# Kernel optimization log

Measured on AMD Instinct MI355X. Metric: run time of the kernel, lower is better.

Reference implementation:

```python
import jax, jax.numpy as jnp
import numpy as np

N = 20000      # nodes
E = 80000      # edges (before self loops)
NG = 64        # graphs in batch
EMB = 780      # embedding_size (768 text + 12 time)
NEG_SLOPE = 0.2
BN_EPS = 1e-5


def setup_inputs() -> dict:
    key = jax.random.key(0)
    ks = jax.random.split(key, 20)
    def rn(k, shape, s=0.05):
        return jax.random.normal(k, shape, dtype=jnp.float32) * s
    z = lambda n: jnp.zeros((n,), dtype=jnp.float32)
    o = lambda n: jnp.ones((n,), dtype=jnp.float32)
    x = jax.random.normal(ks[0], (N, 772), dtype=jnp.float32)
    edge_index = jax.random.randint(ks[1], (2, E), 0, N)
    batch = jnp.sort(jax.random.randint(ks[2], (N,), 0, NG))
    return dict(
        x=x, edge_index=edge_index, batch=batch,
        time_W=rn(ks[3], (4, 12)), time_b=z(12),
        lin_W0=rn(ks[4], (EMB, 3 * EMB)), att_src0=rn(ks[5], (3, EMB)), att_dst0=rn(ks[6], (3, EMB)),
        bias0=z(3 * EMB), gamma0=o(3 * EMB), beta0=z(3 * EMB),
        lin_W1=rn(ks[7], (3 * EMB, 3 * EMB)), att_src1=rn(ks[8], (3, EMB)), att_dst1=rn(ks[9], (3, EMB)),
        bias1=z(3 * EMB), gamma1=o(3 * EMB), beta1=z(3 * EMB),
        lin_W2=rn(ks[10], (3 * EMB, EMB)), att_src2=rn(ks[11], (1, EMB)), att_dst2=rn(ks[12], (1, EMB)),
        bias2=z(EMB), gamma2=o(EMB), beta2=z(EMB),
        mlp_W1=rn(ks[13], (EMB, 128)), mlp_b1=z(128),
        mlp_W2=rn(ks[14], (128, 64)), mlp_b2=z(64),
    )


def _gat_layer(h, src, dst, W, a_src, a_dst, b, heads):
    # PyG GATConv (eval mode: dropout off), concat=True, self loops already in src/dst
    C = W.shape[1] // heads
    hp = (h @ W).reshape(N, heads, C)                       # [N,H,C]
    a_s = jnp.sum(hp * a_src[None], axis=-1)                # [N,H]
    a_d = jnp.sum(hp * a_dst[None], axis=-1)                # [N,H]
    e = jax.nn.leaky_relu(a_s[src] + a_d[dst], NEG_SLOPE)   # [E+N,H]
    m = jax.ops.segment_max(e, dst, num_segments=N)         # segment softmax over incoming edges
    m = jnp.where(jnp.isfinite(m), m, 0.0)
    p = jnp.exp(e - m[dst])
    denom = jax.ops.segment_sum(p, dst, num_segments=N)
    alpha = p / (denom[dst] + 1e-16)                        # [E+N,H]
    out = jax.ops.segment_sum(alpha[:, :, None] * hp[src], dst, num_segments=N)  # [N,H,C]
    return out.reshape(N, heads * C) + b


def _bn(h, gamma, beta):
    # BatchNorm in training-mode math (batch statistics, biased variance)
    mu = jnp.mean(h, axis=0)
    var = jnp.mean((h - mu) ** 2, axis=0)
    return (h - mu) * jax.lax.rsqrt(var + BN_EPS) * gamma + beta


def reference(x, edge_index, batch, time_W, time_b,
              lin_W0, att_src0, att_dst0, bias0, gamma0, beta0,
              lin_W1, att_src1, att_dst1, bias1, gamma1, beta1,
              lin_W2, att_src2, att_dst2, bias2, gamma2, beta2,
              mlp_W1, mlp_b1, mlp_W2, mlp_b2):
    te = x[:, 768:772] @ time_W + time_b
    h = jnp.concatenate([jax.lax.stop_gradient(x[:, :768]), te,
                         jax.lax.stop_gradient(x[:, 772:])], axis=-1)  # [N, 780]
    sl = jnp.arange(N)
    src = jnp.concatenate([edge_index[0], sl])   # add self loops
    dst = jnp.concatenate([edge_index[1], sl])
    layers = [
        (lin_W0, att_src0, att_dst0, bias0, gamma0, beta0, 3),
        (lin_W1, att_src1, att_dst1, bias1, gamma1, beta1, 3),
        (lin_W2, att_src2, att_dst2, bias2, gamma2, beta2, 1),
    ]
    for W, a_s, a_d, b, g, bt, heads in layers:
        h = jnp.tanh(_gat_layer(h, src, dst, W, a_s, a_d, b, heads))
        h = _bn(h, g, bt)
    cnt = jax.ops.segment_sum(jnp.ones((N,), dtype=h.dtype), batch, num_segments=NG)
    pooled = jax.ops.segment_sum(h, batch, num_segments=NG) / jnp.maximum(cnt, 1.0)[:, None]
    pooled = jax.nn.relu(pooled)
    out = jnp.tanh(pooled @ mlp_W1 + mlp_b1) @ mlp_W2 + mlp_b2
    return out  # [NG, 64]
```

## Files before the change

kernel.cpp:

```cpp
#include <hip/hip_runtime.h>
#include <math.h>

#define NN   20000
#define EE   80000
#define ELP  100000
#define NGR  64
#define EMB  780
#define W3   2340
#define EMBP 832
#define W3P  2368

static inline int cdiv_i(long long a, long long b){ return (int)((a + b - 1) / b); }

typedef _Float16 f16;
typedef _Float16 f16x4 __attribute__((ext_vector_type(4)));
typedef _Float16 f16x8 __attribute__((ext_vector_type(8)));
typedef float    f32x4 __attribute__((ext_vector_type(4)));

__device__ __forceinline__ void async_ld16(const f16* g, f16* l){
    __builtin_amdgcn_global_load_lds(
        (const __attribute__((address_space(1))) unsigned int*)g,
        (__attribute__((address_space(3))) unsigned int*)l,
        16, 0, 0);
}

__global__ void k_zero_f32(float* p, int n){
    int i = blockIdx.x*256 + threadIdx.x; if (i < n) p[i] = 0.f;
}
__global__ void k_zero_i32(int* p, int n){
    int i = blockIdx.x*256 + threadIdx.x; if (i < n) p[i] = 0;
}
__global__ void k_copy_i32(const int* __restrict__ s, int* __restrict__ d, int n){
    int i = blockIdx.x*256 + threadIdx.x; if (i < n) d[i] = s[i];
}

__global__ void k_transpose(const float* __restrict__ W, f16* __restrict__ Wt,
                            const float* __restrict__ sc, int K, int N, int KP){
    __shared__ float T[32][33];
    int n0 = blockIdx.x*32, k0 = blockIdx.y*32;
    int tx = threadIdx.x, ty = threadIdx.y;
#pragma unroll
    for (int r = 0; r < 4; r++){
        int k = k0 + ty + r*8;
        float v = 0.f;
        if (k < K && n0 + tx < N){
            v = W[(size_t)k*N + n0 + tx];
            if (sc) v *= sc[k];
        }
        T[ty + r*8][tx] = v;
    }
    __syncthreads();
#pragma unroll
    for (int r = 0; r < 4; r++){
        int n = n0 + ty + r*8;
        int k = k0 + tx;
        if (n < N && k < KP) Wt[(size_t)n*KP + k] = (f16)T[tx][ty + r*8];
    }
}

#define DVEC_KSPLIT 32
__global__ void k_dvec(const float* __restrict__ W, const float* __restrict__ sh,
                       float* __restrict__ dvec, int K, int N){
    int n = blockIdx.x*256 + threadIdx.x;
    if (n >= N) return;
    int slice = blockIdx.y;
    int k0 = (int)(((long long)K * slice) / DVEC_KSPLIT);
    int k1 = (int)(((long long)K * (slice+1)) / DVEC_KSPLIT);
    float s = 0.f;
    for (int k = k0; k < k1; k++) s += sh[k] * W[(size_t)k*N + n];
    atomicAdd(&dvec[n], s);
}

__global__ void k_build_h(const float* __restrict__ x, const float* __restrict__ tW,
                          const float* __restrict__ tb, f16* __restrict__ h){
    int idx = blockIdx.x*256 + threadIdx.x;
    if (idx >= NN*EMBP) return;
    int n = idx / EMBP, c = idx - n*EMBP;
    const float* xr = x + (size_t)n*772;
    float v;
    if (c < 768) v = xr[c];
    else if (c < EMB){
        int j = c - 768;
        v = tb[j] + xr[768]*tW[j] + xr[769]*tW[12+j] + xr[770]*tW[24+j] + xr[771]*tW[36+j];
    } else v = 0.f;
    h[idx] = (f16)v;
}

__global__ void k_deg(const int* __restrict__ ei, int* __restrict__ deg){
    int k = blockIdx.x*256 + threadIdx.x; if (k >= ELP) return;
    int d = (k < EE) ? ei[EE + k] : (k - EE);
    atomicAdd(&deg[d], 1);
}

__global__ __launch_bounds__(1024) void k_scan(const int* __restrict__ deg, int* __restrict__ rp){
    __shared__ int part[1024];
    int tid = threadIdx.x;
    int i0 = tid*20;
    int n = (i0 < NN) ? min(20, NN - i0) : 0;
    int s = 0;
    for (int k = 0; k < n; k++) s += deg[i0+k];
    part[tid] = s; __syncthreads();
    for (int off = 1; off < 1024; off <<= 1){
        int t = (tid >= off) ? part[tid-off] : 0;
        __syncthreads();
        part[tid] += t;
        __syncthreads();
    }
    int run = part[tid] - s;
    for (int k = 0; k < n; k++){ rp[i0+k] = run; run += deg[i0+k]; }
    if (tid == 1023) rp[NN] = part[1023];
}

__global__ void k_fill(const int* __restrict__ ei, int* __restrict__ cursor, int* __restrict__ csrc){
    int k = blockIdx.x*256 + threadIdx.x; if (k >= ELP) return;
    int s, d;
    if (k < EE){ s = ei[k]; d = ei[EE + k]; } else { s = k - EE; d = s; }
    int pos = atomicAdd(&cursor[d], 1);
    csrc[pos] = s;
}

__global__ void k_grp(const int* __restrict__ batch, int* __restrict__ grp){
    int g = blockIdx.x*256 + threadIdx.x; if (g > NGR) return;
    int lo = 0, hi = NN;
    while (lo < hi){ int mid = (lo+hi)>>1; if (batch[mid] < g) lo = mid+1; else hi = mid; }
    grp[g] = lo;
}

__global__ __launch_bounds__(256) void k_gemm_mfma(const f16* __restrict__ A,
                                                   const f16* __restrict__ Bt,
                                                   const float* __restrict__ dvec,
                                                   f16* __restrict__ C,
                                                   int M, int N, int KP, int SN,
                                                   int Mtiles, int NT){
    int bid = blockIdx.x;
    int xcd = bid & 7;
    int j   = bid >> 3;
    int sl  = j / NT;
    int nt  = j - sl*NT;
    int mt  = sl*8 + xcd;
    if (mt >= Mtiles) return;
    int m0 = mt*128, n0 = nt*128;

    __shared__ f16 As[128*64];
    __shared__ f16 Bs[128*64];
    int tid = threadIdx.x;
    int w = tid >> 6, lane = tid & 63;

    int lrow = lane >> 2;
    int lko  = (lane & 3) * 8;

    int i2a = w*2, i2b = w*2 + 1;
    const f16* gA0 = A  + (size_t)min(m0 + i2a*16 + lrow, M-1)*KP + lko;
    const f16* gA1 = A  + (size_t)min(m0 + i2b*16 + lrow, M-1)*KP + lko;
    const f16* gB0 = Bt + (size_t)min(n0 + i2a*16 + lrow, N-1)*KP + lko;
    const f16* gB1 = Bt + (size_t)min(n0 + i2b*16 + lrow, N-1)*KP + lko;
    f16* lA0 = &As[i2a*512]; f16* lA1 = &As[i2b*512];
    f16* lB0 = &Bs[i2a*512]; f16* lB1 = &Bs[i2b*512];

    f32x4 acc[4][4];
#pragma unroll
    for (int i = 0; i < 4; i++)
#pragma unroll
        for (int j2 = 0; j2 < 4; j2++) acc[i][j2] = (f32x4)0.f;

    int wm = (w & 1) * 64, wn = (w >> 1) * 64;
    int lq = lane >> 4, lm = lane & 15;

    for (int kk = 0; kk < KP; kk += 64){
        __syncthreads();
        async_ld16(gA0 + kk, lA0);
        async_ld16(gA1 + kk, lA1);
        async_ld16(gB0 + kk, lB0);
        async_ld16(gB1 + kk, lB1);
        async_ld16(gA0 + kk + 32, lA0 + 4096);
        async_ld16(gA1 + kk + 32, lA1 + 4096);
        async_ld16(gB0 + kk + 32, lB0 + 4096);
        async_ld16(gB1 + kk + 32, lB1 + 4096);
        __syncthreads();

#pragma unroll
        for (int half = 0; half < 2; half++){
            const f16* Ap = As + half*4096;
            const f16* Bp = Bs + half*4096;
            f16x8 aF[4], bF[4];
#pragma unroll
            for (int mi = 0; mi < 4; mi++)
                aF[mi] = *(const f16x8*)&Ap[(wm + mi*16 + lm)*32 + lq*8];
#pragma unroll
            for (int ni = 0; ni < 4; ni++)
                bF[ni] = *(const f16x8*)&Bp[(wn + ni*16 + lm)*32 + lq*8];
#pragma unroll
            for (int mi = 0; mi < 4; mi++)
#pragma unroll
                for (int ni = 0; ni < 4; ni++)
                    acc[mi][ni] = __builtin_amdgcn_mfma_f32_16x16x32_f16(aF[mi], bF[ni], acc[mi][ni], 0, 0, 0);
        }
    }

#pragma unroll
    for (int mi = 0; mi < 4; mi++){
#pragma unroll
        for (int ni = 0; ni < 4; ni++){
            int col = n0 + wn + ni*16 + lm;
            if (col < SN){
                float dv = (col < N) ? dvec[col] : 0.f;
                int rbase = m0 + wm + mi*16 + lq*4;
#pragma unroll
                for (int r = 0; r < 4; r++){
                    int row = rbase + r;
                    if (row < M){
                        float v = (col < N) ? (acc[mi][ni][r] + dv) : 0.f;
                        C[(size_t)row*SN + col] = (f16)v;
                    }
                }
            }
        }
    }
}

__global__ void k_att(const f16* __restrict__ hp, const float* __restrict__ asrc,
                      const float* __restrict__ adst, float* __restrict__ a_s,
                      float* __restrict__ a_d, int H, int SP){
    int n = blockIdx.x;
    int wv = threadIdx.x >> 6, lane = threadIdx.x & 63;
    const f16* row = hp + (size_t)n*SP + wv*EMB;
    const float* pa = asrc + wv*EMB;
    const float* pd = adst + wv*EMB;
    float s = 0.f, d = 0.f;
    for (int c = lane*4; c < EMB; c += 256){
        f16x4 v = *(const f16x4*)(row + c);
#pragma unroll
        for (int jj = 0; jj < 4; jj++){
            float f = (float)v[jj];
            s += f*pa[c+jj]; d += f*pd[c+jj];
        }
    }
#pragma unroll
    for (int off = 32; off; off >>= 1){ s += __shfl_xor(s, off); d += __shfl_xor(d, off); }
    if (lane == 0){ a_s[n*H + wv] = s; a_d[n*H + wv] = d; }
}

template<int H>
__global__ __launch_bounds__(256) void k_agg2(const f16* __restrict__ hp, const int* __restrict__ rp,
                                              const int* __restrict__ csrc, const float* __restrict__ a_s,
                                              const float* __restrict__ a_d, const float* __restrict__ bias,
                                              f16* __restrict__ y, int SP, int W){
    int n = blockIdx.x, tid = threadIdx.x, lane = tid & 63;
    int beg = rp[n], deg = rp[n+1] - beg;

    float adv[H];
#pragma unroll
    for (int h = 0; h < H; h++) adv[h] = a_d[n*H + h];

    float mx[H];
#pragma unroll
    for (int h = 0; h < H; h++) mx[h] = -1e30f;
    for (int base = 0; base < deg; base += 64){
        int e = base + lane;
        if (e < deg){
            int s = csrc[beg + e];
#pragma unroll
            for (int h = 0; h < H; h++){
                float t = a_s[s*H + h] + adv[h];
                t = t > 0.f ? t : 0.2f*t;
                mx[h] = fmaxf(mx[h], t);
            }
        }
    }
#pragma unroll
    for (int off = 32; off; off >>= 1)
#pragma unroll
        for (int h = 0; h < H; h++) mx[h] = fmaxf(mx[h], __shfl_xor(mx[h], off));

    float dn[H];
#pragma unroll
    for (int h = 0; h < H; h++) dn[h] = 0.f;
    for (int base = 0; base < deg; base += 64){
        int e = base + lane;
        if (e < deg){
            int s = csrc[beg + e];
#pragma unroll
            for (int h = 0; h < H; h++){
                float t = a_s[s*H + h] + adv[h];
                t = t > 0.f ? t : 0.2f*t;
                dn[h] += expf(t - mx[h]);
            }
        }
    }
#pragma unroll
    for (int off = 32; off; off >>= 1)
#pragma unroll
        for (int h = 0; h < H; h++) dn[h] += __shfl_xor(dn[h], off);
    float inv[H];
#pragma unroll
    for (int h = 0; h < H; h++) inv[h] = 1.f / (dn[h] + 1e-16f);

    float acc[2][8];
#pragma unroll
    for (int g = 0; g < 2; g++)
#pragma unroll
        for (int j = 0; j < 8; j++) acc[g][j] = 0.f;
    int  cg[2];  cg[0] = tid*8; cg[1] = 2048 + tid*8;
    bool act[2]; act[0] = cg[0] < W; act[1] = cg[1] < W;
    int hlo[2], hhi[2], nsp[2];
#pragma unroll
    for (int g = 0; g < 2; g++){
        int c = cg[g];
        int hl = min(c / EMB, H-1);
        int hh = min((c+7) / EMB, H-1);
        hlo[g] = hl; hhi[g] = hh;
        nsp[g] = (hh > hl) ? (EMB*(hl+1) - c) : 8;
    }

    for (int base = 0; base < deg; base += 64){
        int cnt = min(64, deg - base);
        int sl = 0; float al[H];
        {
            int e = base + lane;
            if (e < deg){
                sl = csrc[beg + e];
#pragma unroll
                for (int h = 0; h < H; h++){
                    float t = a_s[sl*H + h] + adv[h];
                    t = t > 0.f ? t : 0.2f*t;
                    al[h] = expf(t - mx[h]) * inv[h];
                }
            } else {
#pragma unroll
                for (int h = 0; h < H; h++) al[h] = 0.f;
            }
        }
#pragma unroll 2
        for (int e = 0; e < cnt; e++){
            int s = __shfl(sl, e);
            float a0 = __shfl(al[0], e);
            float a1 = (H==3) ? __shfl(al[1], e) : a0;
            float a2 = (H==3) ? __shfl(al[2], e) : a0;
            const f16* row = hp + (size_t)s*SP;
#pragma unroll
            for (int g = 0; g < 2; g++){
                if (act[g]){
                    f16x8 v = *(const f16x8*)(row + cg[g]);
                    float lo = (hlo[g]==0) ? a0 : (hlo[g]==1 ? a1 : a2);
                    float hi = (hhi[g]==0) ? a0 : (hhi[g]==1 ? a1 : a2);
#pragma unroll
                    for (int j = 0; j < 8; j++){
                        float alj = (j < nsp[g]) ? lo : hi;
                        acc[g][j] += alj * (float)v[j];
                    }
                }
            }
        }
    }

#pragma unroll
    for (int g = 0; g < 2; g++){
        int c = cg[g];
        if (c < SP){
            f16x8 o;
#pragma unroll
            for (int j = 0; j < 8; j++){
                float vv = (c + j < W) ? tanhf(acc[g][j] + bias[c+j]) : 0.f;
                o[j] = (f16)vv;
            }
            *(f16x8*)(y + (size_t)n*SP + c) = o;
        }
    }
}

__global__ void k_bnstat(const f16* __restrict__ y, float* __restrict__ ps,
                         float* __restrict__ pq, int W, int SP){
    int c0 = (blockIdx.x*256 + threadIdx.x)*4;
    if (c0 >= W) return;
    int slice = blockIdx.y;
    float s[4] = {0,0,0,0}, q[4] = {0,0,0,0};
    for (int r = slice; r < NN; r += 64){
        f16x4 u = *(const f16x4*)(y + (size_t)r*SP + c0);
#pragma unroll
        for (int j = 0; j < 4; j++){ float v = (float)u[j]; s[j] += v; q[j] += v*v; }
    }
#pragma unroll
    for (int j = 0; j < 4; j++){
        ps[(size_t)slice*W3 + c0+j] = s[j];
        pq[(size_t)slice*W3 + c0+j] = q[j];
    }
}

__global__ void k_bnfin(const float* __restrict__ ps, const float* __restrict__ pq,
                        const float* __restrict__ gamma, const float* __restrict__ beta,
                        float* __restrict__ sc, float* __restrict__ sh, int W){
    int c = blockIdx.x*256 + threadIdx.x; if (c >= W) return;
    float m = 0.f, q = 0.f;
    for (int s = 0; s < 64; s++){ m += ps[(size_t)s*W3 + c]; q += pq[(size_t)s*W3 + c]; }
    m *= (1.f/NN);
    float v = q * (1.f/NN) - m*m;
    float is = 1.f / sqrtf(v + 1e-5f);
    float g = gamma[c];
    sc[c] = is * g;
    sh[c] = beta[c] - m * is * g;
}

__global__ void k_pool(const f16* __restrict__ h, const int* __restrict__ grp,
                       float* __restrict__ pooled){
    int g = blockIdx.x;
    int c = threadIdx.x*4;
    if (c >= EMB) return;
    int r0 = grp[g], r1 = grp[g+1];
    float s0=0.f, s1=0.f, s2=0.f, s3=0.f;
    for (int r = r0; r < r1; r++){
        f16x4 u = *(const f16x4*)(h + (size_t)r*EMBP + c);
        s0 += (float)u[0]; s1 += (float)u[1]; s2 += (float)u[2]; s3 += (float)u[3];
    }
    pooled[g*EMB + c] = s0; pooled[g*EMB + c+1] = s1;
    pooled[g*EMB + c+2] = s2; pooled[g*EMB + c+3] = s3;
}

__global__ __launch_bounds__(256) void k_mlp(const float* __restrict__ pooled, const int* __restrict__ grp,
                                             const float* __restrict__ sc, const float* __restrict__ sh,
                                             const float* __restrict__ W1, const float* __restrict__ b1,
                                             const float* __restrict__ W2, const float* __restrict__ b2,
                                             float* __restrict__ out){
    __shared__ float p[EMB];
    __shared__ float hid[128];
    int g = blockIdx.x, tid = threadIdx.x;
    int cnt = grp[g+1] - grp[g];
    float ic = 1.f / fmaxf((float)cnt, 1.f);
    for (int c = tid; c < EMB; c += 256){
        float v = pooled[g*EMB + c] * ic * sc[c] + sh[c];
        p[c] = v > 0.f ? v : 0.f;
    }
    __syncthreads();
    if (tid < 128){
        float s = b1[tid];
        for (int k = 0; k < EMB; k++) s += p[k] * W1[k*128 + tid];
        hid[tid] = tanhf(s);
    }
    __syncthreads();
    if (tid < 64){
        float s = b2[tid];
        for (int k = 0; k < 128; k++) s += hid[k] * W2[k*64 + tid];
        out[g*64 + tid] = s;
    }
}

extern "C" void kernel_launch(void* const* d_in, const int* in_sizes, int n_in,
                              void* d_out, int out_size, void* d_ws, size_t ws_size,
                              hipStream_t stream) {
    (void)in_sizes; (void)n_in; (void)out_size;
    const float* x    = (const float*)d_in[0];
    const int*   ei   = (const int*)  d_in[1];
    const int*   batch= (const int*)  d_in[2];
    const float* tW   = (const float*)d_in[3];
    const float* tb   = (const float*)d_in[4];
    const float* W0   = (const float*)d_in[5];
    const float* as0  = (const float*)d_in[6];
    const float* ad0  = (const float*)d_in[7];
    const float* b0   = (const float*)d_in[8];
    const float* g0   = (const float*)d_in[9];
    const float* be0  = (const float*)d_in[10];
    const float* W1   = (const float*)d_in[11];
    const float* as1  = (const float*)d_in[12];
    const float* ad1  = (const float*)d_in[13];
    const float* b1   = (const float*)d_in[14];
    const float* g1   = (const float*)d_in[15];
    const float* be1  = (const float*)d_in[16];
    const float* W2   = (const float*)d_in[17];
    const float* as2  = (const float*)d_in[18];
    const float* ad2  = (const float*)d_in[19];
    const float* b2   = (const float*)d_in[20];
    const float* g2   = (const float*)d_in[21];
    const float* be2  = (const float*)d_in[22];
    const float* mW1  = (const float*)d_in[23];
    const float* mb1  = (const float*)d_in[24];
    const float* mW2  = (const float*)d_in[25];
    const float* mb2  = (const float*)d_in[26];
    float* outp = (float*)d_out;

    size_t off = 0;
    auto carve = [&](size_t bytes) -> void* {
        void* p = (char*)d_ws + off;
        off = (off + bytes + 255) & ~(size_t)255;
        return p;
    };
    f16* big1 = (f16*)carve((size_t)NN*W3P*2);
    f16* big2 = (f16*)carve((size_t)NN*W3P*2);
    f16* Wt   = (f16*)carve((size_t)W3*W3P*2);
    float* a_s   = (float*)carve((size_t)NN*3*4);
    float* a_d   = (float*)carve((size_t)NN*3*4);
    float* psum  = (float*)carve((size_t)64*W3*4);
    float* psq   = (float*)carve((size_t)64*W3*4);
    float* sc    = (float*)carve((size_t)W3*4);
    float* sh    = (float*)carve((size_t)W3*4);
    float* dvec  = (float*)carve((size_t)W3*4);
    float* pooled= (float*)carve((size_t)NGR*EMB*4);
    int*   grp   = (int*)carve((size_t)(NGR+1)*4);
    int*   deg   = (int*)carve((size_t)NN*4);
    int*   rp    = (int*)carve((size_t)(NN+1)*4);
    int*   csrc  = (int*)carve((size_t)ELP*4);

    if (ws_size < off) return;

    k_zero_i32<<<cdiv_i(NN,256),256,0,stream>>>(deg, NN);
    k_deg<<<cdiv_i(ELP,256),256,0,stream>>>(ei, deg);
    k_scan<<<1,1024,0,stream>>>(deg, rp);
    k_copy_i32<<<cdiv_i(NN,256),256,0,stream>>>(rp, deg, NN);
    k_fill<<<cdiv_i(ELP,256),256,0,stream>>>(ei, deg, csrc);
    k_grp<<<1,256,0,stream>>>(batch, grp);

    k_build_h<<<cdiv_i((long long)NN*EMBP,256),256,0,stream>>>(x, tW, tb, big1);

    struct Layer { const float* W; const float* as; const float* ad; const float* b;
                   const float* g; const float* be; int H; int K; int KP; };
    Layer layers[3] = {
        {W0, as0, ad0, b0, g0, be0, 3, EMB, EMBP},
        {W1, as1, ad1, b1, g1, be1, 3, W3,  W3P },
        {W2, as2, ad2, b2, g2, be2, 1, W3,  W3P },
    };

    for (int L = 0; L < 3; L++){
        Layer& ly = layers[L];
        int Wout  = ly.H * EMB;
        int SPout = (Wout == W3) ? W3P : EMBP;
        const float* scale = (L == 0) ? nullptr : sc;

        dim3 tg(cdiv_i(Wout,32), cdiv_i(ly.KP,32));
        k_transpose<<<tg, dim3(32,8), 0, stream>>>(ly.W, Wt, scale, ly.K, Wout, ly.KP);
        k_zero_f32<<<cdiv_i(W3,256),256,0,stream>>>(dvec, W3);
        if (L > 0){
            dim3 dg(cdiv_i(Wout,256), DVEC_KSPLIT);
            k_dvec<<<dg,256,0,stream>>>(ly.W, sh, dvec, ly.K, Wout);
        }

        int Mtiles = cdiv_i(NN,128), NT = cdiv_i(Wout,128);
        int nb = ((Mtiles+7)/8)*8*NT;
        k_gemm_mfma<<<nb, 256, 0, stream>>>(big1, Wt, dvec, big2, NN, Wout, ly.KP, SPout, Mtiles, NT);

        k_att<<<NN, ly.H*64, 0, stream>>>(big2, ly.as, ly.ad, a_s, a_d, ly.H, SPout);

        if (ly.H == 3)
            k_agg2<3><<<NN,256,0,stream>>>(big2, rp, csrc, a_s, a_d, ly.b, big1, SPout, Wout);
        else
            k_agg2<1><<<NN,256,0,stream>>>(big2, rp, csrc, a_s, a_d, ly.b, big1, SPout, Wout);

        dim3 gs(cdiv_i(Wout/4,256), 64);
        k_bnstat<<<gs,256,0,stream>>>(big1, psum, psq, Wout, SPout);
        k_bnfin<<<cdiv_i(Wout,256),256,0,stream>>>(psum, psq, ly.g, ly.be, sc, sh, Wout);
    }

    k_pool<<<NGR,256,0,stream>>>(big1, grp, pooled);
    k_mlp<<<NGR,256,0,stream>>>(pooled, grp, sc, sh, mW1, mb1, mW2, mb2, outp);
}
```

Before: 1.678 ms.

## Fold attention score projections into the GEMM as extra output columns

Precomputes W·a_src and W·a_dst vectors, including the BN scale, and appends them as extra rows of the transposed weight. The main MFMA GEMM then emits the per-node attention logits directly into a compact a_sd buffer, and the separate k_att pass that re-read the whole projected feature matrix is removed. The BN shift contribution is added through extended dvec entries computed by a tiny k_wfin kernel. The BN-stat row split also goes from 64 to 128 slices, and dvec zeroing is merged into k_bnfin. The attention logits now come from f16-rounded weight vectors instead of dot products over the stored features, which slightly changes precision.

```diff
diff --git a/kernel.cpp b/kernel.cpp
--- a/kernel.cpp
+++ b/kernel.cpp
@@ -9,6 +9,7 @@
 #define W3   2340
 #define EMBP 832
 #define W3P  2368
+#define NZ   (W3+8)
 
 static inline int cdiv_i(long long a, long long b){ return (int)((a + b - 1) / b); }
 
@@ -55,6 +56,46 @@
         int n = n0 + ty + r*8;
         int k = k0 + tx;
         if (n < N && k < KP) Wt[(size_t)n*KP + k] = (f16)T[tx][ty + r*8];
+    }
+}
+
+__global__ void k_wvec(const float* __restrict__ W, const float* __restrict__ asrc,
+                       const float* __restrict__ adst, const float* __restrict__ sc,
+                       f16* __restrict__ Wt, int K, int N, int KP, int H){
+    int k = blockIdx.x*4 + (threadIdx.x >> 6);
+    int lane = threadIdx.x & 63;
+    if (k >= K) return;
+    const float* row = W + (size_t)k*N;
+    float acc[6];
+#pragma unroll
+    for (int i = 0; i < 6; i++) acc[i] = 0.f;
+    for (int c = lane; c < EMB; c += 64){
+        for (int h = 0; h < H; h++){
+            float wv = row[h*EMB + c];
+            acc[h]     += wv * asrc[h*EMB + c];
+            acc[H + h] += wv * adst[h*EMB + c];
+        }
+    }
+    float s = sc ? sc[k] : 1.f;
+    for (int i = 0; i < 2*H; i++){
+        float v = acc[i];
+#pragma unroll
+        for (int off = 32; off; off >>= 1) v += __shfl_xor(v, off);
+        if (lane == 0) Wt[(size_t)(N + i)*KP + k] = (f16)(v * s);
+    }
+}
+
+__global__ void k_wfin(const float* __restrict__ asrc, const float* __restrict__ adst,
+                       float* __restrict__ dvec, int N, int H){
+    int wv = threadIdx.x >> 6, lane = threadIdx.x & 63;
+    for (int i = wv; i < 2*H; i += 4){
+        int h = (i < H) ? i : (i - H);
+        const float* att = (i < H) ? (asrc + h*EMB) : (adst + h*EMB);
+        float s = 0.f;
+        for (int c = lane; c < EMB; c += 64) s += dvec[h*EMB + c] * att[c];
+#pragma unroll
+        for (int off = 32; off; off >>= 1) s += __shfl_xor(s, off);
+        if (lane == 0) dvec[N + i] = s;
     }
 }
 
@@ -130,7 +171,9 @@
                                                    const f16* __restrict__ Bt,
                                                    const float* __restrict__ dvec,
                                                    f16* __restrict__ C,
-                                                   int M, int N, int KP, int SN,
+                                                   float* __restrict__ a_sd,
+                                                   int M, int N, int NB, int H,
+                                                   int KP, int SN,
                                                    int Mtiles, int NT){
     int bid = blockIdx.x;
     int xcd = bid & 7;
@@ -152,8 +195,8 @@
     int i2a = w*2, i2b = w*2 + 1;
     const f16* gA0 = A  + (size_t)min(m0 + i2a*16 + lrow, M-1)*KP + lko;
     const f16* gA1 = A  + (size_t)min(m0 + i2b*16 + lrow, M-1)*KP + lko;
-    const f16* gB0 = Bt + (size_t)min(n0 + i2a*16 + lrow, N-1)*KP + lko;
-    const f16* gB1 = Bt + (size_t)min(n0 + i2b*16 + lrow, N-1)*KP + lko;
+    const f16* gB0 = Bt + (size_t)min(n0 + i2a*16 + lrow, NB-1)*KP + lko;
+    const f16* gB1 = Bt + (size_t)min(n0 + i2b*16 + lrow, NB-1)*KP + lko;
     f16* lA0 = &As[i2a*512]; f16* lA1 = &As[i2b*512];
     f16* lB0 = &Bs[i2a*512]; f16* lB1 = &Bs[i2b*512];
 
@@ -202,55 +245,41 @@
 #pragma unroll
         for (int ni = 0; ni < 4; ni++){
             int col = n0 + wn + ni*16 + lm;
-            if (col < SN){
-                float dv = (col < N) ? dvec[col] : 0.f;
-                int rbase = m0 + wm + mi*16 + lq*4;
+            int rbase = m0 + wm + mi*16 + lq*4;
+            if (col < N){
+                float dv = dvec[col];
 #pragma unroll
                 for (int r = 0; r < 4; r++){
                     int row = rbase + r;
-                    if (row < M){
-                        float v = (col < N) ? (acc[mi][ni][r] + dv) : 0.f;
-                        C[(size_t)row*SN + col] = (f16)v;
-                    }
+                    if (row < M)
+                        C[(size_t)row*SN + col] = (f16)(acc[mi][ni][r] + dv);
+                }
+            } else if (col < NB){
+                int jc = col - N;
+                int idx = (jc < H) ? jc : (3 + jc - H);
+                float dv = dvec[col];
+#pragma unroll
+                for (int r = 0; r < 4; r++){
+                    int row = rbase + r;
+                    if (row < M)
+                        a_sd[(size_t)row*6 + idx] = acc[mi][ni][r] + dv;
                 }
             }
         }
     }
 }
 
-__global__ void k_att(const f16* __restrict__ hp, const float* __restrict__ asrc,
-                      const float* __restrict__ adst, float* __restrict__ a_s,
-                      float* __restrict__ a_d, int H, int SP){
-    int n = blockIdx.x;
-    int wv = threadIdx.x >> 6, lane = threadIdx.x & 63;
-    const f16* row = hp + (size_t)n*SP + wv*EMB;
-    const float* pa = asrc + wv*EMB;
-    const float* pd = adst + wv*EMB;
-    float s = 0.f, d = 0.f;
-    for (int c = lane*4; c < EMB; c += 256){
-        f16x4 v = *(const f16x4*)(row + c);
-#pragma unroll
-        for (int jj = 0; jj < 4; jj++){
-            float f = (float)v[jj];
-            s += f*pa[c+jj]; d += f*pd[c+jj];
-        }
-    }
-#pragma unroll
-    for (int off = 32; off; off >>= 1){ s += __shfl_xor(s, off); d += __shfl_xor(d, off); }
-    if (lane == 0){ a_s[n*H + wv] = s; a_d[n*H + wv] = d; }
-}
-
 template<int H>
 __global__ __launch_bounds__(256) void k_agg2(const f16* __restrict__ hp, const int* __restrict__ rp,
-                                              const int* __restrict__ csrc, const float* __restrict__ a_s,
-                                              const float* __restrict__ a_d, const float* __restrict__ bias,
+                                              const int* __restrict__ csrc, const float* __restrict__ a_sd,
+                                              const float* __restrict__ bias,
                                               f16* __restrict__ y, int SP, int W){
     int n = blockIdx.x, tid = threadIdx.x, lane = tid & 63;
     int beg = rp[n], deg = rp[n+1] - beg;
 
     float adv[H];
 #pragma unroll
-    for (int h = 0; h < H; h++) adv[h] = a_d[n*H + h];
+    for (int h = 0; h < H; h++) adv[h] = a_sd[(size_t)n*6 + 3 + h];
 
     float mx[H];
 #pragma unroll
@@ -261,7 +290,7 @@
             int s = csrc[beg + e];
 #pragma unroll
             for (int h = 0; h < H; h++){
-                float t = a_s[s*H + h] + adv[h];
+                float t = a_sd[(size_t)s*6 + h] + adv[h];
                 t = t > 0.f ? t : 0.2f*t;
                 mx[h] = fmaxf(mx[h], t);
             }
@@ -281,7 +310,7 @@
             int s = csrc[beg + e];
 #pragma unroll
             for (int h = 0; h < H; h++){
-                float t = a_s[s*H + h] + adv[h];
+                float t = a_sd[(size_t)s*6 + h] + adv[h];
                 t = t > 0.f ? t : 0.2f*t;
                 dn[h] += expf(t - mx[h]);
             }
@@ -321,7 +350,7 @@
                 sl = csrc[beg + e];
 #pragma unroll
                 for (int h = 0; h < H; h++){
-                    float t = a_s[sl*H + h] + adv[h];
+                    float t = a_sd[(size_t)sl*6 + h] + adv[h];
                     t = t > 0.f ? t : 0.2f*t;
                     al[h] = expf(t - mx[h]) * inv[h];
                 }
@@ -374,7 +403,7 @@
     if (c0 >= W) return;
     int slice = blockIdx.y;
     float s[4] = {0,0,0,0}, q[4] = {0,0,0,0};
-    for (int r = slice; r < NN; r += 64){
+    for (int r = slice; r < NN; r += 128){
         f16x4 u = *(const f16x4*)(y + (size_t)r*SP + c0);
 #pragma unroll
         for (int j = 0; j < 4; j++){ float v = (float)u[j]; s[j] += v; q[j] += v*v; }
@@ -388,16 +417,20 @@
 
 __global__ void k_bnfin(const float* __restrict__ ps, const float* __restrict__ pq,
                         const float* __restrict__ gamma, const float* __restrict__ beta,
-                        float* __restrict__ sc, float* __restrict__ sh, int W){
-    int c = blockIdx.x*256 + threadIdx.x; if (c >= W) return;
-    float m = 0.f, q = 0.f;
-    for (int s = 0; s < 64; s++){ m += ps[(size_t)s*W3 + c]; q += pq[(size_t)s*W3 + c]; }
-    m *= (1.f/NN);
-    float v = q * (1.f/NN) - m*m;
-    float is = 1.f / sqrtf(v + 1e-5f);
-    float g = gamma[c];
-    sc[c] = is * g;
-    sh[c] = beta[c] - m * is * g;
+                        float* __restrict__ sc, float* __restrict__ sh,
+                        float* __restrict__ dvec, int W, int zn){
+    int c = blockIdx.x*256 + threadIdx.x;
+    if (c < W){
+        float m = 0.f, q = 0.f;
+        for (int s = 0; s < 128; s++){ m += ps[(size_t)s*W3 + c]; q += pq[(size_t)s*W3 + c]; }
+        m *= (1.f/NN);
+        float v = q * (1.f/NN) - m*m;
+        float is = 1.f / sqrtf(v + 1e-5f);
+        float g = gamma[c];
+        sc[c] = is * g;
+        sh[c] = beta[c] - m * is * g;
+    }
+    if (c < zn) dvec[c] = 0.f;
 }
 
 __global__ void k_pool(const f16* __restrict__ h, const int* __restrict__ grp,
@@ -484,14 +517,13 @@
     };
     f16* big1 = (f16*)carve((size_t)NN*W3P*2);
     f16* big2 = (f16*)carve((size_t)NN*W3P*2);
-    f16* Wt   = (f16*)carve((size_t)W3*W3P*2);
-    float* a_s   = (float*)carve((size_t)NN*3*4);
-    float* a_d   = (float*)carve((size_t)NN*3*4);
-    float* psum  = (float*)carve((size_t)64*W3*4);
-    float* psq   = (float*)carve((size_t)64*W3*4);
+    f16* Wt   = (f16*)carve((size_t)NZ*W3P*2);
+    float* a_sd  = (float*)carve((size_t)NN*6*4);
+    float* psum  = (float*)carve((size_t)128*W3*4);
+    float* psq   = (float*)carve((size_t)128*W3*4);
     float* sc    = (float*)carve((size_t)W3*4);
     float* sh    = (float*)carve((size_t)W3*4);
-    float* dvec  = (float*)carve((size_t)W3*4);
+    float* dvec  = (float*)carve((size_t)NZ*4);
     float* pooled= (float*)carve((size_t)NGR*EMB*4);
     int*   grp   = (int*)carve((size_t)(NGR+1)*4);
     int*   deg   = (int*)carve((size_t)NN*4);
@@ -508,6 +540,7 @@
     k_grp<<<1,256,0,stream>>>(batch, grp);
 
     k_build_h<<<cdiv_i((long long)NN*EMBP,256),256,0,stream>>>(x, tW, tb, big1);
+    k_zero_f32<<<cdiv_i(NZ,256),256,0,stream>>>(dvec, NZ);
 
     struct Layer { const float* W; const float* as; const float* ad; const float* b;
                    const float* g; const float* be; int H; int K; int KP; };
@@ -520,31 +553,33 @@
     for (int L = 0; L < 3; L++){
         Layer& ly = layers[L];
         int Wout  = ly.H * EMB;
+        int NB    = Wout + 2*ly.H;
         int SPout = (Wout == W3) ? W3P : EMBP;
         const float* scale = (L == 0) ? nullptr : sc;
 
         dim3 tg(cdiv_i(Wout,32), cdiv_i(ly.KP,32));
         k_transpose<<<tg, dim3(32,8), 0, stream>>>(ly.W, Wt, scale, ly.K, Wout, ly.KP);
-        k_zero_f32<<<cdiv_i(W3,256),256,0,stream>>>(dvec, W3);
+        k_wvec<<<cdiv_i(ly.K,4),256,0,stream>>>(ly.W, ly.as, ly.ad, scale, Wt, ly.K, Wout, ly.KP, ly.H);
         if (L > 0){
             dim3 dg(cdiv_i(Wout,256), DVEC_KSPLIT);
             k_dvec<<<dg,256,0,stream>>>(ly.W, sh, dvec, ly.K, Wout);
         }
-
-        int Mtiles = cdiv_i(NN,128), NT = cdiv_i(Wout,128);
+        k_wfin<<<1,256,0,stream>>>(ly.as, ly.ad, dvec, Wout, ly.H);
+
+        int Mtiles = cdiv_i(NN,128), NT = cdiv_i(NB,128);
         int nb = ((Mtiles+7)/8)*8*NT;
-        k_gemm_mfma<<<nb, 256, 0, stream>>>(big1, Wt, dvec, big2, NN, Wout, ly.KP, SPout, Mtiles, NT);
-
-        k_att<<<NN, ly.H*64, 0, stream>>>(big2, ly.as, ly.ad, a_s, a_d, ly.H, SPout);
+        k_gemm_mfma<<<nb, 256, 0, stream>>>(big1, Wt, dvec, big2, a_sd,
+                                            NN, Wout, NB, ly.H, ly.KP, SPout, Mtiles, NT);
 
         if (ly.H == 3)
-            k_agg2<3><<<NN,256,0,stream>>>(big2, rp, csrc, a_s, a_d, ly.b, big1, SPout, Wout);
+            k_agg2<3><<<NN,256,0,stream>>>(big2, rp, csrc, a_sd, ly.b, big1, SPout, Wout);
         else
-            k_agg2<1><<<NN,256,0,stream>>>(big2, rp, csrc, a_s, a_d, ly.b, big1, SPout, Wout);
-
-        dim3 gs(cdiv_i(Wout/4,256), 64);
+            k_agg2<1><<<NN,256,0,stream>>>(big2, rp, csrc, a_sd, ly.b, big1, SPout, Wout);
+
+        dim3 gs(cdiv_i(Wout/4,256), 128);
         k_bnstat<<<gs,256,0,stream>>>(big1, psum, psq, Wout, SPout);
-        k_bnfin<<<cdiv_i(Wout,256),256,0,stream>>>(psum, psq, ly.g, ly.be, sc, sh, Wout);
+        int zn = (L < 2) ? NZ : 0;
+        k_bnfin<<<cdiv_i(Wout,256),256,0,stream>>>(psum, psq, ly.g, ly.be, sc, sh, dvec, Wout, zn);
     }
 
     k_pool<<<NGR,256,0,stream>>>(big1, grp, pooled);
```

New measurement: 1.651 ms. No clear change (-1.6%).
